# Kernel optimization log

Measured on AMD Instinct MI355X. Metric: run time of the kernel, lower is better.

Reference implementation:

```python
import jax, jax.numpy as jnp
import numpy as np

B, S, D, H = 2, 2048, 768, 12
DK = D // H
DF = 3072
SOFTCAP = 30.0
LN_EPS = 1e-5
NEG_INF = -1e30


def layer_norm(x, g, b):
    m = jnp.mean(x, axis=-1, keepdims=True)
    v = jnp.mean(jnp.square(x - m), axis=-1, keepdims=True)
    return (x - m) * jax.lax.rsqrt(v + LN_EPS) * g + b


def setup_inputs() -> dict:
    key = jax.random.key(0)
    ks = jax.random.split(key, 12)
    s = 0.02
    x = jax.random.normal(ks[0], (B, S, D), jnp.float32)
    count_bias = jax.random.normal(ks[1], (B, 1, S, S), jnp.float32)
    # causal mask: True = allowed
    attn_mask = jnp.broadcast_to(jnp.tril(jnp.ones((S, S), bool)), (B, 1, S, S))
    Wq = jax.random.normal(ks[2], (D, D), jnp.float32) * s
    Wk = jax.random.normal(ks[3], (D, D), jnp.float32) * s
    Wv = jax.random.normal(ks[4], (D, D), jnp.float32) * s
    Wo = jax.random.normal(ks[5], (D, D), jnp.float32) * s
    W1 = jax.random.normal(ks[6], (D, DF), jnp.float32) * s
    W2 = jax.random.normal(ks[7], (DF, D), jnp.float32) * s
    g1 = jnp.ones((D,), jnp.float32)
    b1 = jnp.zeros((D,), jnp.float32)
    g2 = jnp.ones((D,), jnp.float32)
    b2 = jnp.zeros((D,), jnp.float32)
    return dict(x=x, count_bias=count_bias, attn_mask=attn_mask, Wq=Wq, Wk=Wk,
                Wv=Wv, Wo=Wo, W1=W1, W2=W2, g1=g1, b1=b1, g2=g2, b2=b2)


def reference(x, count_bias, attn_mask, Wq, Wk, Wv, Wo, W1, W2, g1, b1, g2, b2):
    # pre-norm (note: residual taken from normed activations, faithful to source)
    h = layer_norm(x, g1, b1)                                   # (B,S,D)
    q = (h @ Wq).reshape(B, S, H, DK).transpose(0, 2, 1, 3)     # (B,H,S,DK)
    k = (h @ Wk).reshape(B, S, H, DK).transpose(0, 2, 1, 3)
    v = (h @ Wv).reshape(B, S, H, DK).transpose(0, 2, 1, 3)
    scale = 1.0 / np.sqrt(DK).astype(np.float32)
    scores = jnp.einsum('bhqd,bhkd->bhqk', q, k) * scale + count_bias
    scores = jnp.tanh(scores / SOFTCAP) * SOFTCAP               # softcap
    scores = jnp.where(attn_mask, scores, NEG_INF)
    weights = jax.nn.softmax(scores, axis=-1)
    o = jnp.einsum('bhqk,bhkd->bhqd', weights, v)               # (B,H,S,DK)
    o = o.transpose(0, 2, 1, 3).reshape(B, S, D) @ Wo
    x1 = o + h
    h2 = layer_norm(x1, g2, b2)
    ffn = jax.nn.gelu(h2 @ W1, approximate=False) @ W2
    return ffn + h2
```

## Files before the change

kernel.cpp:

```cpp
#include <hip/hip_runtime.h>
#include <hip/hip_bf16.h>
#include <cstdint>

#define Bn 2
#define Sn 2048
#define Dn 768
#define Hn 12
#define DKn 64
#define DFn 3072
#define Mrows 4096

typedef float f32x4 __attribute__((ext_vector_type(4)));
typedef __bf16 bf16x8 __attribute__((ext_vector_type(8)));
typedef short s16x8 __attribute__((ext_vector_type(8)));
typedef short s16x4 __attribute__((ext_vector_type(4)));

__device__ __forceinline__ f32x4 MFMA(s16x8 a, s16x8 b, f32x4 c) {
  return __builtin_amdgcn_mfma_f32_16x16x32_bf16(
      __builtin_bit_cast(bf16x8, a), __builtin_bit_cast(bf16x8, b), c, 0, 0, 0);
}

__device__ __forceinline__ void g2lds16(const void* g, void* l) {
  __builtin_amdgcn_global_load_lds(
      (__attribute__((address_space(1))) void*)(g),
      (__attribute__((address_space(3))) void*)(l), 16, 0, 0);
}

__device__ __forceinline__ short f2bf(float f) {
  unsigned u = __builtin_bit_cast(unsigned, f);
  unsigned r = (u + 0x7fffu + ((u >> 16) & 1u)) >> 16;
  return (short)r;
}

__global__ void wtrans(const float* __restrict__ in, short* __restrict__ out, int R, int C) {
  __shared__ float t[32][33];
  int c0 = blockIdx.x * 32, r0 = blockIdx.y * 32;
  int tx = threadIdx.x, ty = threadIdx.y;
#pragma unroll
  for (int i = 0; i < 4; i++) t[ty + i * 8][tx] = in[(size_t)(r0 + ty + i * 8) * C + c0 + tx];
  __syncthreads();
#pragma unroll
  for (int i = 0; i < 4; i++) out[(size_t)(c0 + ty + i * 8) * R + r0 + tx] = f2bf(t[tx][ty + i * 8]);
}

__global__ __launch_bounds__(256) void ln_kernel(const float* __restrict__ x,
                                                 const float* __restrict__ g,
                                                 const float* __restrict__ b,
                                                 short* __restrict__ hb,
                                                 float* __restrict__ hf) {
  int row = blockIdx.x;
  const float* xr = x + (size_t)row * Dn;
  int tid = threadIdx.x;
  float v[3];
  float s = 0.f, ss = 0.f;
#pragma unroll
  for (int i = 0; i < 3; i++) {
    v[i] = xr[tid + i * 256];
    s += v[i];
    ss += v[i] * v[i];
  }
#pragma unroll
  for (int m = 1; m < 64; m <<= 1) {
    s += __shfl_xor(s, m);
    ss += __shfl_xor(ss, m);
  }
  __shared__ float red[8];
  int w = tid >> 6, lane = tid & 63;
  if (lane == 0) { red[w] = s; red[4 + w] = ss; }
  __syncthreads();
  s = red[0] + red[1] + red[2] + red[3];
  ss = red[4] + red[5] + red[6] + red[7];
  float mean = s * (1.0f / Dn);
  float var = ss * (1.0f / Dn) - mean * mean;
  float rs = rsqrtf(var + 1e-5f);
#pragma unroll
  for (int i = 0; i < 3; i++) {
    int c = tid + i * 256;
    float h = (v[i] - mean) * rs * g[c] + b[c];
    hb[(size_t)row * Dn + c] = f2bf(h);
    hf[(size_t)row * Dn + c] = h;
  }
}

template <int EPI>
__global__ __launch_bounds__(256) void gemm_bt(const short* __restrict__ A,
                                               const short* __restrict__ Bt,
                                               short* __restrict__ Cb,
                                               const float* __restrict__ addm,
                                               float* __restrict__ Cf,
                                               int M, int N, int K) {
  __shared__ __align__(16) short As[4096];
  __shared__ __align__(16) short Bs[4096];
  int tid = threadIdx.x;
  int lane = tid & 63, w = tid >> 6, g = lane >> 4, lt = lane & 15;
  int wr = w >> 1, wc = w & 1;
  int m0 = blockIdx.x * 128, n0 = blockIdx.y * 128;
  int sr = tid >> 2, su = (tid & 3) * 8;
  const short* Ag = A + (size_t)(m0 + sr) * K + su;
  const short* Bg = Bt + (size_t)(n0 + sr) * K + su;
  f32x4 acc[4][4] = {};
  for (int k0 = 0; k0 < K; k0 += 32) {
    g2lds16(Ag + k0, &As[tid * 8]);
    g2lds16(Ag + k0 + (size_t)64 * K, &As[2048 + tid * 8]);
    g2lds16(Bg + k0, &Bs[tid * 8]);
    g2lds16(Bg + k0 + (size_t)64 * K, &Bs[2048 + tid * 8]);
    __syncthreads();
    s16x8 af[4], bfr[4];
#pragma unroll
    for (int i = 0; i < 4; i++) {
      af[i] = *(const s16x8*)&As[(wr * 64 + i * 16 + lt) * 32 + g * 8];
      bfr[i] = *(const s16x8*)&Bs[(wc * 64 + i * 16 + lt) * 32 + g * 8];
    }
#pragma unroll
    for (int mi = 0; mi < 4; mi++)
#pragma unroll
      for (int ni = 0; ni < 4; ni++) acc[mi][ni] = MFMA(af[mi], bfr[ni], acc[mi][ni]);
    __syncthreads();
  }
#pragma unroll
  for (int mi = 0; mi < 4; mi++) {
    int m = m0 + wr * 64 + mi * 16 + g * 4;
#pragma unroll
    for (int ni = 0; ni < 4; ni++) {
      int n = n0 + wc * 64 + ni * 16 + lt;
#pragma unroll
      for (int r = 0; r < 4; r++) {
        float v = acc[mi][ni][r];
        size_t idx = (size_t)(m + r) * N + n;
        if constexpr (EPI == 0) {
          Cb[idx] = f2bf(v);
        } else if constexpr (EPI == 1) {
          float ge = 0.5f * v * (1.0f + erff(v * 0.70710678f));
          Cb[idx] = f2bf(ge);
        } else {
          Cf[idx] = v + addm[idx];
        }
      }
    }
  }
}

template <int EPI>
__global__ __launch_bounds__(256, 4) void gemm64(const short* __restrict__ A,
                                                 const short* __restrict__ Bt,
                                                 short* __restrict__ Cb,
                                                 const float* __restrict__ addm,
                                                 float* __restrict__ Cf,
                                                 int M, int N, int K) {
  __shared__ __align__(16) short As[2][4096];
  __shared__ __align__(16) short Bs[2][4096];
  int tid = threadIdx.x, lane = tid & 63, w = tid >> 6, g = lane >> 4, lt = lane & 15;
  int wr = w >> 1, wc = w & 1;
  int m0 = blockIdx.x * 64, n0 = blockIdx.y * 64;
  int r0 = tid >> 3, cc = (tid & 7) ^ (r0 & 7);
  const short* asrc0 = A + (size_t)(m0 + r0) * K + cc * 8;
  const short* asrc1 = A + (size_t)(m0 + r0 + 32) * K + cc * 8;
  const short* bsrc0 = Bt + (size_t)(n0 + r0) * K + cc * 8;
  const short* bsrc1 = Bt + (size_t)(n0 + r0 + 32) * K + cc * 8;
  int sw = lt & 7;
  int ch0 = (g ^ sw) * 8, ch1 = ((4 + g) ^ sw) * 8;
  f32x4 acc[2][2] = {};
  g2lds16(asrc0, &As[0][tid * 8]);
  g2lds16(asrc1, &As[0][2048 + tid * 8]);
  g2lds16(bsrc0, &Bs[0][tid * 8]);
  g2lds16(bsrc1, &Bs[0][2048 + tid * 8]);
  __syncthreads();
  int nsteps = K >> 6;
  for (int t = 0; t < nsteps; t++) {
    int cur = t & 1;
    if (t + 1 < nsteps) {
      int k0 = (t + 1) << 6;
      g2lds16(asrc0 + k0, &As[cur ^ 1][tid * 8]);
      g2lds16(asrc1 + k0, &As[cur ^ 1][2048 + tid * 8]);
      g2lds16(bsrc0 + k0, &Bs[cur ^ 1][tid * 8]);
      g2lds16(bsrc1 + k0, &Bs[cur ^ 1][2048 + tid * 8]);
    }
    s16x8 af[2][2], bf[2][2];
#pragma unroll
    for (int mi = 0; mi < 2; mi++) {
      af[mi][0] = *(const s16x8*)&As[cur][(wr * 32 + mi * 16 + lt) * 64 + ch0];
      af[mi][1] = *(const s16x8*)&As[cur][(wr * 32 + mi * 16 + lt) * 64 + ch1];
    }
#pragma unroll
    for (int ni = 0; ni < 2; ni++) {
      bf[ni][0] = *(const s16x8*)&Bs[cur][(wc * 32 + ni * 16 + lt) * 64 + ch0];
      bf[ni][1] = *(const s16x8*)&Bs[cur][(wc * 32 + ni * 16 + lt) * 64 + ch1];
    }
#pragma unroll
    for (int mi = 0; mi < 2; mi++)
#pragma unroll
      for (int ni = 0; ni < 2; ni++) {
        acc[mi][ni] = MFMA(af[mi][0], bf[ni][0], acc[mi][ni]);
        acc[mi][ni] = MFMA(af[mi][1], bf[ni][1], acc[mi][ni]);
      }
    __syncthreads();
  }
#pragma unroll
  for (int mi = 0; mi < 2; mi++) {
    int m = m0 + wr * 32 + mi * 16 + g * 4;
#pragma unroll
    for (int ni = 0; ni < 2; ni++) {
      int n = n0 + wc * 32 + ni * 16 + lt;
#pragma unroll
      for (int r = 0; r < 4; r++) {
        float v = acc[mi][ni][r];
        size_t idx = (size_t)(m + r) * N + n;
        if constexpr (EPI == 0) {
          Cb[idx] = f2bf(v);
        } else if constexpr (EPI == 1) {
          float ge = 0.5f * v * (1.0f + erff(v * 0.70710678f));
          Cb[idx] = f2bf(ge);
        } else {
          Cf[idx] = v + addm[idx];
        }
      }
    }
  }
}

__global__ void vtrans(const short* __restrict__ qkv, short* __restrict__ vt) {
  __shared__ short t[32][33];
  int bh = blockIdx.z;
  int b = bh / Hn, h = bh % Hn;
  int s0 = blockIdx.x * 32, d0 = blockIdx.y * 32;
  int tx = threadIdx.x, ty = threadIdx.y;
#pragma unroll
  for (int i = 0; i < 4; i++)
    t[ty + i * 8][tx] =
        qkv[(size_t)(b * Sn + s0 + ty + i * 8) * (3 * Dn) + 2 * Dn + h * DKn + d0 + tx];
  __syncthreads();
#pragma unroll
  for (int i = 0; i < 4; i++)
    vt[(size_t)(bh * DKn + d0 + ty + i * 8) * Sn + s0 + tx] = t[tx][ty + i * 8];
}

__global__ __launch_bounds__(256, 3) void attn_kernel(const short* __restrict__ qkv,
                                                      const short* __restrict__ vt,
                                                      const float* __restrict__ bias,
                                                      short* __restrict__ o) {
  __shared__ __align__(16) short Ks[2][4096];
  __shared__ __align__(16) short Vs[2][4096];
  __shared__ __align__(16) short plds[4][16][72];
  int bh = blockIdx.x;
  int by = blockIdx.y;
  int qt = (by & 1) ? (31 - (by >> 1)) : (by >> 1);
  int b = bh / Hn, h = bh - b * Hn;
  int tid = threadIdx.x, w = tid >> 6, lane = tid & 63, g = lane >> 4, lt = lane & 15;
  int q0 = qt * 64 + w * 16;
  const short* qbase = qkv + (size_t)(b * Sn + q0 + lt) * (3 * Dn) + h * DKn;
  s16x8 qf0 = *(const s16x8*)(qbase + g * 8);
  s16x8 qf1 = *(const s16x8*)(qbase + 32 + g * 8);
  int sr0 = tid >> 3, scc = (tid & 7) ^ (sr0 & 7);
  const short* kseg = qkv + (size_t)b * Sn * (3 * Dn) + Dn + h * DKn;
  const short* ksrc0 = kseg + (size_t)sr0 * (3 * Dn) + scc * 8;
  const short* ksrc1 = kseg + (size_t)(sr0 + 32) * (3 * Dn) + scc * 8;
  const short* vseg = vt + (size_t)bh * DKn * Sn;
  const short* vsrc0 = vseg + (size_t)sr0 * Sn + scc * 8;
  const short* vsrc1 = vseg + (size_t)(sr0 + 32) * Sn + scc * 8;
  int sw = lt & 7;
  int ch0 = (g ^ sw) * 8, ch1 = ((4 + g) ^ sw) * 8;
  const float* biasrow = bias + ((size_t)b * Sn + q0 + g * 4) * Sn;
  const float C1 = 0.0120224586f;
  const float C2 = 0.0961796722f;
  const float C3 = -86.5617013f;
  f32x4 oacc[4] = {};
  float lsum[4] = {0.f, 0.f, 0.f, 0.f};
  g2lds16(ksrc0, &Ks[0][tid * 8]);
  g2lds16(ksrc1, &Ks[0][2048 + tid * 8]);
  g2lds16(vsrc0, &Vs[0][tid * 8]);
  g2lds16(vsrc1, &Vs[0][2048 + tid * 8]);
  __syncthreads();
  for (int t = 0; t <= qt; t++) {
    int cur = t & 1;
    int kc0 = t * 64;
    if (t < qt) {
      size_t koff = (size_t)(kc0 + 64) * (3 * Dn);
      g2lds16(ksrc0 + koff, &Ks[cur ^ 1][tid * 8]);
      g2lds16(ksrc1 + koff, &Ks[cur ^ 1][2048 + tid * 8]);
      g2lds16(vsrc0 + kc0 + 64, &Vs[cur ^ 1][tid * 8]);
      g2lds16(vsrc1 + kc0 + 64, &Vs[cur ^ 1][2048 + tid * 8]);
    }
    float bb[4][4];
#pragma unroll
    for (int c = 0; c < 4; c++)
#pragma unroll
      for (int r = 0; r < 4; r++)
        bb[c][r] = biasrow[(size_t)r * Sn + kc0 + c * 16 + lt] * C2;
    s16x8 kf[4][2];
#pragma unroll
    for (int c = 0; c < 4; c++) {
      kf[c][0] = *(const s16x8*)&Ks[cur][(c * 16 + lt) * 64 + ch0];
      kf[c][1] = *(const s16x8*)&Ks[cur][(c * 16 + lt) * 64 + ch1];
    }
    f32x4 s[4] = {};
#pragma unroll
    for (int c = 0; c < 4; c++) {
      s[c] = MFMA(qf0, kf[c][0], s[c]);
      s[c] = MFMA(qf1, kf[c][1], s[c]);
    }
    s16x8 vf[4][2];
#pragma unroll
    for (int dt = 0; dt < 4; dt++) {
      vf[dt][0] = *(const s16x8*)&Vs[cur][(dt * 16 + lt) * 64 + ch0];
      vf[dt][1] = *(const s16x8*)&Vs[cur][(dt * 16 + lt) * 64 + ch1];
    }
    bool needmask = (t == qt);
#pragma unroll
    for (int c = 0; c < 4; c++) {
#pragma unroll
      for (int r = 0; r < 4; r++) {
        float targ = fmaf(s[c][r], C1, bb[c][r]);
        float e = __builtin_amdgcn_exp2f(targ);
        float u = __builtin_amdgcn_rcpf(1.0f + e);
        float p = __builtin_amdgcn_exp2f(C3 * u);
        if (needmask) p = (kc0 + c * 16 + lt <= q0 + g * 4 + r) ? p : 0.0f;
        lsum[r] += p;
        plds[w][g * 4 + r][c * 16 + lt] = f2bf(p);
      }
    }
    s16x8 pf0 = *(const s16x8*)&plds[w][lt][g * 8];
    s16x8 pf1 = *(const s16x8*)&plds[w][lt][32 + g * 8];
#pragma unroll
    for (int dt = 0; dt < 4; dt++) {
      oacc[dt] = MFMA(pf0, vf[dt][0], oacc[dt]);
      oacc[dt] = MFMA(pf1, vf[dt][1], oacc[dt]);
    }
    __syncthreads();
  }
  float inv[4];
#pragma unroll
  for (int r = 0; r < 4; r++) {
    float l = lsum[r];
    l += __shfl_xor(l, 1);
    l += __shfl_xor(l, 2);
    l += __shfl_xor(l, 4);
    l += __shfl_xor(l, 8);
    inv[r] = __builtin_amdgcn_rcpf(l);
  }
  short* obase = o + (size_t)(b * Sn + q0 + g * 4) * Dn + h * DKn + lt;
#pragma unroll
  for (int dt = 0; dt < 4; dt++)
#pragma unroll
    for (int r = 0; r < 4; r++) obase[(size_t)r * Dn + dt * 16] = f2bf(oacc[dt][r] * inv[r]);
}

extern "C" void kernel_launch(void* const* d_in, const int* in_sizes, int n_in,
                              void* d_out, int out_size, void* d_ws, size_t ws_size,
                              hipStream_t stream) {
  const float* x = (const float*)d_in[0];
  const float* bias = (const float*)d_in[1];
  const float* Wq = (const float*)d_in[3];
  const float* Wk = (const float*)d_in[4];
  const float* Wv = (const float*)d_in[5];
  const float* Wo = (const float*)d_in[6];
  const float* W1 = (const float*)d_in[7];
  const float* W2 = (const float*)d_in[8];
  const float* g1 = (const float*)d_in[9];
  const float* b1 = (const float*)d_in[10];
  const float* g2 = (const float*)d_in[11];
  const float* b2 = (const float*)d_in[12];
  float* out = (float*)d_out;
  char* ws = (char*)d_ws;

  short* wqkv_t = (short*)(ws + 0);
  short* wo_t = (short*)(ws + 3538944);
  short* w1_t = (short*)(ws + 4718592);
  short* w2_t = (short*)(ws + 9437184);
  short* hb = (short*)(ws + 14155776);
  float* hf = (float*)(ws + 20447232);
  short* qkv = (short*)(ws + 33030144);
  short* a1 = qkv;
  short* vt = (short*)(ws + 58195968);
  float* x1 = (float*)(ws + 58195968);
  short* o_ = (short*)(ws + 70778880);
  short* h2b = hb;
  float* h2f = hf;

  dim3 tb(32, 8);
  wtrans<<<dim3(24, 24), tb, 0, stream>>>(Wq, wqkv_t, Dn, Dn);
  wtrans<<<dim3(24, 24), tb, 0, stream>>>(Wk, wqkv_t + (size_t)Dn * Dn, Dn, Dn);
  wtrans<<<dim3(24, 24), tb, 0, stream>>>(Wv, wqkv_t + (size_t)2 * Dn * Dn, Dn, Dn);
  wtrans<<<dim3(24, 24), tb, 0, stream>>>(Wo, wo_t, Dn, Dn);
  wtrans<<<dim3(96, 24), tb, 0, stream>>>(W1, w1_t, Dn, DFn);
  wtrans<<<dim3(24, 96), tb, 0, stream>>>(W2, w2_t, DFn, Dn);

  ln_kernel<<<Mrows, 256, 0, stream>>>(x, g1, b1, hb, hf);

  gemm_bt<0><<<dim3(32, 18), 256, 0, stream>>>(hb, wqkv_t, qkv, nullptr, nullptr,
                                               Mrows, 3 * Dn, Dn);
  vtrans<<<dim3(64, 2, Bn * Hn), tb, 0, stream>>>(qkv, vt);
  attn_kernel<<<dim3(24, 32), 256, 0, stream>>>(qkv, vt, bias, o_);

  gemm64<2><<<dim3(64, 12), 256, 0, stream>>>(o_, wo_t, nullptr, hf, x1,
                                              Mrows, Dn, Dn);
  ln_kernel<<<Mrows, 256, 0, stream>>>(x1, g2, b2, h2b, h2f);
  gemm_bt<1><<<dim3(32, 24), 256, 0, stream>>>(h2b, w1_t, a1, nullptr, nullptr,
                                               Mrows, DFn, Dn);
  gemm64<2><<<dim3(64, 12), 256, 0, stream>>>(a1, w2_t, nullptr, h2f, out,
                                              Mrows, Dn, DFn);
}
```

Before: 335.1 us.

## Precompute bf16 masked bias, prefetch it in attention, double-buffer GEMM with BK=64

Adds a bias_prep kernel that scales the count bias, applies the causal mask as -1e30, and writes it as bf16. Attention then reads half the bias bytes, prefetches the next tile's bias into registers, and drops the per-element mask branch. The main GEMM moves to a double-buffered, XOR-swizzled LDS pipeline with a 64-wide K step, and the three QKV weight transposes merge into one launch. Costs: an extra full pass over the bias each call, more LDS per GEMM block, and bf16 rounding of the bias.

```diff
diff --git a/kernel.cpp b/kernel.cpp
--- a/kernel.cpp
+++ b/kernel.cpp
@@ -32,6 +32,31 @@
   return (short)r;
 }
 
+__device__ __forceinline__ float bf2f(short s) {
+  unsigned u = ((unsigned)(unsigned short)s) << 16;
+  return __builtin_bit_cast(float, u);
+}
+
+#define C1f 0.0120224586f
+#define C2f 0.0961796722f
+#define C3f -86.5617013f
+
+__global__ __launch_bounds__(256) void bias_prep(const float* __restrict__ bias,
+                                                 short* __restrict__ biasb) {
+  int gid = blockIdx.x * 256 + threadIdx.x;
+  size_t i8 = (size_t)gid * 8;
+  int q = (int)((i8 >> 11) & 2047);
+  int k0 = (int)(i8 & 2047);
+  f32x4 v0 = *(const f32x4*)(bias + i8);
+  f32x4 v1 = *(const f32x4*)(bias + i8 + 4);
+  s16x8 o;
+#pragma unroll
+  for (int j = 0; j < 4; j++) o[j] = (k0 + j <= q) ? f2bf(v0[j] * C2f) : f2bf(-1e30f);
+#pragma unroll
+  for (int j = 0; j < 4; j++) o[4 + j] = (k0 + 4 + j <= q) ? f2bf(v1[j] * C2f) : f2bf(-1e30f);
+  *(s16x8*)(biasb + i8) = o;
+}
+
 __global__ void wtrans(const float* __restrict__ in, short* __restrict__ out, int R, int C) {
   __shared__ float t[32][33];
   int c0 = blockIdx.x * 32, r0 = blockIdx.y * 32;
@@ -41,6 +66,21 @@
   __syncthreads();
 #pragma unroll
   for (int i = 0; i < 4; i++) out[(size_t)(c0 + ty + i * 8) * R + r0 + tx] = f2bf(t[tx][ty + i * 8]);
+}
+
+__global__ void wtrans3(const float* __restrict__ Wq, const float* __restrict__ Wk,
+                        const float* __restrict__ Wv, short* __restrict__ out) {
+  __shared__ float t[32][33];
+  int z = blockIdx.z;
+  const float* in = (z == 0) ? Wq : (z == 1) ? Wk : Wv;
+  short* o = out + (size_t)z * Dn * Dn;
+  int c0 = blockIdx.x * 32, r0 = blockIdx.y * 32;
+  int tx = threadIdx.x, ty = threadIdx.y;
+#pragma unroll
+  for (int i = 0; i < 4; i++) t[ty + i * 8][tx] = in[(size_t)(r0 + ty + i * 8) * Dn + c0 + tx];
+  __syncthreads();
+#pragma unroll
+  for (int i = 0; i < 4; i++) o[(size_t)(c0 + ty + i * 8) * Dn + r0 + tx] = f2bf(t[tx][ty + i * 8]);
 }
 
 __global__ __launch_bounds__(256) void ln_kernel(const float* __restrict__ x,
@@ -83,38 +123,67 @@
 }
 
 template <int EPI>
-__global__ __launch_bounds__(256) void gemm_bt(const short* __restrict__ A,
-                                               const short* __restrict__ Bt,
-                                               short* __restrict__ Cb,
-                                               const float* __restrict__ addm,
-                                               float* __restrict__ Cf,
-                                               int M, int N, int K) {
-  __shared__ __align__(16) short As[4096];
-  __shared__ __align__(16) short Bs[4096];
-  int tid = threadIdx.x;
-  int lane = tid & 63, w = tid >> 6, g = lane >> 4, lt = lane & 15;
+__global__ __launch_bounds__(256, 2) void gemm_bt(const short* __restrict__ A,
+                                                  const short* __restrict__ Bt,
+                                                  short* __restrict__ Cb,
+                                                  const float* __restrict__ addm,
+                                                  float* __restrict__ Cf,
+                                                  int M, int N, int K) {
+  __shared__ __align__(16) short As[2][8192];
+  __shared__ __align__(16) short Bs[2][8192];
+  int tid = threadIdx.x, lane = tid & 63, w = tid >> 6, g = lane >> 4, lt = lane & 15;
   int wr = w >> 1, wc = w & 1;
   int m0 = blockIdx.x * 128, n0 = blockIdx.y * 128;
-  int sr = tid >> 2, su = (tid & 3) * 8;
-  const short* Ag = A + (size_t)(m0 + sr) * K + su;
-  const short* Bg = Bt + (size_t)(n0 + sr) * K + su;
+  int r0 = tid >> 3, c8 = tid & 7;
+  const short* Ags[4];
+  const short* Bgs[4];
+#pragma unroll
+  for (int h = 0; h < 4; h++) {
+    int row = h * 32 + r0;
+    int cc = c8 ^ (row & 7);
+    Ags[h] = A + (size_t)(m0 + row) * K + cc * 8;
+    Bgs[h] = Bt + (size_t)(n0 + row) * K + cc * 8;
+  }
+  int sw = lt & 7;
+  int ch0 = (g ^ sw) * 8, ch1 = ((4 + g) ^ sw) * 8;
   f32x4 acc[4][4] = {};
-  for (int k0 = 0; k0 < K; k0 += 32) {
-    g2lds16(Ag + k0, &As[tid * 8]);
-    g2lds16(Ag + k0 + (size_t)64 * K, &As[2048 + tid * 8]);
-    g2lds16(Bg + k0, &Bs[tid * 8]);
-    g2lds16(Bg + k0 + (size_t)64 * K, &Bs[2048 + tid * 8]);
-    __syncthreads();
-    s16x8 af[4], bfr[4];
+#pragma unroll
+  for (int h = 0; h < 4; h++) {
+    g2lds16(Ags[h], &As[0][(h * 256 + tid) * 8]);
+    g2lds16(Bgs[h], &Bs[0][(h * 256 + tid) * 8]);
+  }
+  __syncthreads();
+  int nsteps = K >> 6;
+  for (int t = 0; t < nsteps; t++) {
+    int cur = t & 1;
+    if (t + 1 < nsteps) {
+      int k0 = (t + 1) << 6;
+#pragma unroll
+      for (int h = 0; h < 4; h++) {
+        g2lds16(Ags[h] + k0, &As[cur ^ 1][(h * 256 + tid) * 8]);
+        g2lds16(Bgs[h] + k0, &Bs[cur ^ 1][(h * 256 + tid) * 8]);
+      }
+    }
+    s16x8 af[4][2], bf[4][2];
 #pragma unroll
     for (int i = 0; i < 4; i++) {
-      af[i] = *(const s16x8*)&As[(wr * 64 + i * 16 + lt) * 32 + g * 8];
-      bfr[i] = *(const s16x8*)&Bs[(wc * 64 + i * 16 + lt) * 32 + g * 8];
+      int row = wr * 64 + i * 16 + lt;
+      af[i][0] = *(const s16x8*)&As[cur][row * 64 + ch0];
+      af[i][1] = *(const s16x8*)&As[cur][row * 64 + ch1];
+    }
+#pragma unroll
+    for (int i = 0; i < 4; i++) {
+      int row = wc * 64 + i * 16 + lt;
+      bf[i][0] = *(const s16x8*)&Bs[cur][row * 64 + ch0];
+      bf[i][1] = *(const s16x8*)&Bs[cur][row * 64 + ch1];
     }
 #pragma unroll
     for (int mi = 0; mi < 4; mi++)
 #pragma unroll
-      for (int ni = 0; ni < 4; ni++) acc[mi][ni] = MFMA(af[mi], bfr[ni], acc[mi][ni]);
+      for (int ni = 0; ni < 4; ni++) {
+        acc[mi][ni] = MFMA(af[mi][0], bf[ni][0], acc[mi][ni]);
+        acc[mi][ni] = MFMA(af[mi][1], bf[ni][1], acc[mi][ni]);
+      }
     __syncthreads();
   }
 #pragma unroll
@@ -236,7 +305,7 @@
 
 __global__ __launch_bounds__(256, 3) void attn_kernel(const short* __restrict__ qkv,
                                                       const short* __restrict__ vt,
-                                                      const float* __restrict__ bias,
+                                                      const short* __restrict__ biasb,
                                                       short* __restrict__ o) {
   __shared__ __align__(16) short Ks[2][4096];
   __shared__ __align__(16) short Vs[2][4096];
@@ -259,16 +328,18 @@
   const short* vsrc1 = vseg + (size_t)(sr0 + 32) * Sn + scc * 8;
   int sw = lt & 7;
   int ch0 = (g ^ sw) * 8, ch1 = ((4 + g) ^ sw) * 8;
-  const float* biasrow = bias + ((size_t)b * Sn + q0 + g * 4) * Sn;
-  const float C1 = 0.0120224586f;
-  const float C2 = 0.0961796722f;
-  const float C3 = -86.5617013f;
+  const short* bbase = biasb + ((size_t)b * Sn + q0 + g * 4) * Sn + lt;
   f32x4 oacc[4] = {};
   float lsum[4] = {0.f, 0.f, 0.f, 0.f};
   g2lds16(ksrc0, &Ks[0][tid * 8]);
   g2lds16(ksrc1, &Ks[0][2048 + tid * 8]);
   g2lds16(vsrc0, &Vs[0][tid * 8]);
   g2lds16(vsrc1, &Vs[0][2048 + tid * 8]);
+  short sb[16];
+#pragma unroll
+  for (int c = 0; c < 4; c++)
+#pragma unroll
+    for (int r = 0; r < 4; r++) sb[c * 4 + r] = bbase[(size_t)r * Sn + c * 16];
   __syncthreads();
   for (int t = 0; t <= qt; t++) {
     int cur = t & 1;
@@ -280,12 +351,14 @@
       g2lds16(vsrc0 + kc0 + 64, &Vs[cur ^ 1][tid * 8]);
       g2lds16(vsrc1 + kc0 + 64, &Vs[cur ^ 1][2048 + tid * 8]);
     }
-    float bb[4][4];
-#pragma unroll
-    for (int c = 0; c < 4; c++)
-#pragma unroll
-      for (int r = 0; r < 4; r++)
-        bb[c][r] = biasrow[(size_t)r * Sn + kc0 + c * 16 + lt] * C2;
+    short sbn[16];
+    if (t < qt) {
+      int kn = kc0 + 64;
+#pragma unroll
+      for (int c = 0; c < 4; c++)
+#pragma unroll
+        for (int r = 0; r < 4; r++) sbn[c * 4 + r] = bbase[(size_t)r * Sn + kn + c * 16];
+    }
     s16x8 kf[4][2];
 #pragma unroll
     for (int c = 0; c < 4; c++) {
@@ -304,16 +377,14 @@
       vf[dt][0] = *(const s16x8*)&Vs[cur][(dt * 16 + lt) * 64 + ch0];
       vf[dt][1] = *(const s16x8*)&Vs[cur][(dt * 16 + lt) * 64 + ch1];
     }
-    bool needmask = (t == qt);
 #pragma unroll
     for (int c = 0; c < 4; c++) {
 #pragma unroll
       for (int r = 0; r < 4; r++) {
-        float targ = fmaf(s[c][r], C1, bb[c][r]);
+        float targ = fmaf(s[c][r], C1f, bf2f(sb[c * 4 + r]));
         float e = __builtin_amdgcn_exp2f(targ);
         float u = __builtin_amdgcn_rcpf(1.0f + e);
-        float p = __builtin_amdgcn_exp2f(C3 * u);
-        if (needmask) p = (kc0 + c * 16 + lt <= q0 + g * 4 + r) ? p : 0.0f;
+        float p = __builtin_amdgcn_exp2f(C3f * u);
         lsum[r] += p;
         plds[w][g * 4 + r][c * 16 + lt] = f2bf(p);
       }
@@ -326,6 +397,10 @@
       oacc[dt] = MFMA(pf1, vf[dt][1], oacc[dt]);
     }
     __syncthreads();
+    if (t < qt) {
+#pragma unroll
+      for (int i = 0; i < 16; i++) sb[i] = sbn[i];
+    }
   }
   float inv[4];
 #pragma unroll
@@ -373,13 +448,13 @@
   short* vt = (short*)(ws + 58195968);
   float* x1 = (float*)(ws + 58195968);
   short* o_ = (short*)(ws + 70778880);
+  short* biasb = (short*)(ws + 77070336);
   short* h2b = hb;
   float* h2f = hf;
 
   dim3 tb(32, 8);
-  wtrans<<<dim3(24, 24), tb, 0, stream>>>(Wq, wqkv_t, Dn, Dn);
-  wtrans<<<dim3(24, 24), tb, 0, stream>>>(Wk, wqkv_t + (size_t)Dn * Dn, Dn, Dn);
-  wtrans<<<dim3(24, 24), tb, 0, stream>>>(Wv, wqkv_t + (size_t)2 * Dn * Dn, Dn, Dn);
+  bias_prep<<<4096, 256, 0, stream>>>(bias, biasb);
+  wtrans3<<<dim3(24, 24, 3), tb, 0, stream>>>(Wq, Wk, Wv, wqkv_t);
   wtrans<<<dim3(24, 24), tb, 0, stream>>>(Wo, wo_t, Dn, Dn);
   wtrans<<<dim3(96, 24), tb, 0, stream>>>(W1, w1_t, Dn, DFn);
   wtrans<<<dim3(24, 96), tb, 0, stream>>>(W2, w2_t, DFn, Dn);
@@ -389,7 +464,7 @@
   gemm_bt<0><<<dim3(32, 18), 256, 0, stream>>>(hb, wqkv_t, qkv, nullptr, nullptr,
                                                Mrows, 3 * Dn, Dn);
   vtrans<<<dim3(64, 2, Bn * Hn), tb, 0, stream>>>(qkv, vt);
-  attn_kernel<<<dim3(24, 32), 256, 0, stream>>>(qkv, vt, bias, o_);
+  attn_kernel<<<dim3(24, 32), 256, 0, stream>>>(qkv, vt, biasb, o_);
 
   gemm64<2><<<dim3(64, 12), 256, 0, stream>>>(o_, wo_t, nullptr, hf, x1,
                                               Mrows, Dn, Dn);
```

New measurement: 339.9 us. Within noise of the previous version (+1.4%).
